# Optimization experiments

Hardware: AMD Instinct MI355X
Metric: run time of the kernel (lower is better)

## Reference

```python
import jax, jax.numpy as jnp
import numpy as np

V, M, E, H = 20000, 32, 128, 4      # vocab, max news per word, embed dim, heads
N, L, C = 8192, 64, 128             # num news, max sent len, cnn out channels
KS = (3, 4, 5)


def setup_inputs() -> dict:
    key = jax.random.key(0)
    ks = jax.random.split(key, 12)
    s = 0.02
    return {
        "word2news": jax.random.randint(ks[0], (V, M), 0, N),
        "word2news_len": jax.random.randint(ks[1], (V,), 0, M),
        "news_words": jax.random.randint(ks[2], (N, L), 0, V),
        "news_embed_table": jax.random.normal(ks[3], (N, E), jnp.float32) * s,
        "in_proj_w": jax.random.normal(ks[4], (3 * E, E), jnp.float32) * s,
        "in_proj_b": jnp.zeros((3 * E,), jnp.float32),
        "out_proj_w": jax.random.normal(ks[5], (E, E), jnp.float32) * s,
        "out_proj_b": jnp.zeros((E,), jnp.float32),
        "conv_w3": jax.random.normal(ks[6], (C, E, 3), jnp.float32) * s,
        "conv_b3": jnp.zeros((C,), jnp.float32),
        "conv_w4": jax.random.normal(ks[7], (C, E, 4), jnp.float32) * s,
        "conv_b4": jnp.zeros((C,), jnp.float32),
        "conv_w5": jax.random.normal(ks[8], (C, E, 5), jnp.float32) * s,
        "conv_b5": jnp.zeros((C,), jnp.float32),
        "fc_w": jax.random.normal(ks[9], (E, len(KS) * C), jnp.float32) * s,
        "fc_b": jnp.zeros((E,), jnp.float32),
    }


def _conv1d(x, w, b):
    # x: [N, E, L]  w: [C, E, k]  -> [N, C, L-k+1]
    y = jax.lax.conv_general_dilated(x, w, (1,), "VALID",
                                     dimension_numbers=("NCH", "OIH", "NCH"))
    return y + b[None, :, None]


def _word_embeds(word2news, word2news_len, table, in_w, in_b, out_w, out_b):
    # Batched version of the per-word loop: masked mean query + 1-query MHA.
    mask = jnp.arange(M)[None, :] < word2news_len[:, None]          # [V, M]
    ctx = table[word2news]                                           # [V, M, E]
    cnt = jnp.maximum(word2news_len, 1).astype(ctx.dtype)[:, None]
    q = jnp.sum(jnp.where(mask[:, :, None], ctx, 0.0), axis=1) / cnt  # [V, E]
    wq, wk, wv = jnp.split(in_w, 3, axis=0)
    bq, bk, bv = jnp.split(in_b, 3, axis=0)
    Dh = E // H
    qh = (q @ wq.T + bq).reshape(V, H, Dh)
    kh = (ctx @ wk.T + bk).reshape(V, M, H, Dh)
    vh = (ctx @ wv.T + bv).reshape(V, M, H, Dh)
    scores = jnp.einsum("vhd,vmhd->vhm", qh, kh) / jnp.sqrt(jnp.asarray(Dh, ctx.dtype))
    scores = jnp.where(mask[:, None, :], scores, -1e9)
    attn = jax.nn.softmax(scores, axis=-1)
    o = jnp.einsum("vhm,vmhd->vhd", attn, vh).reshape(V, E)
    o = o @ out_w.T + out_b
    # words with no news stay zero, matching the zeros-init table in torch
    return jnp.where((word2news_len > 0)[:, None], o, 0.0)            # [V, E]


def reference(word2news, word2news_len, news_words, news_embed_table,
              in_proj_w, in_proj_b, out_proj_w, out_proj_b,
              conv_w3, conv_b3, conv_w4, conv_b4, conv_w5, conv_b5,
              fc_w, fc_b):
    word_embeds = _word_embeds(word2news, word2news_len, news_embed_table,
                               in_proj_w, in_proj_b, out_proj_w, out_proj_b)
    doc = word_embeds[news_words]                 # [N, L, E]
    x = doc.transpose(0, 2, 1)                    # [N, E, L]
    pooled = [jnp.max(jax.nn.relu(_conv1d(x, w, b)), axis=2)
              for w, b in ((conv_w3, conv_b3), (conv_w4, conv_b4), (conv_w5, conv_b5))]
    feats = jnp.concatenate(pooled, axis=1)       # [N, 3*C]; dropout=identity (eval)
    return feats @ fc_w.T + fc_b                  # [N, E]
```

## Files before the change

kernel.cpp:

```cpp
#include <hip/hip_runtime.h>
#include <math.h>

#define V_WORDS 20000
#define MM 32
#define EE 128
#define HH 4
#define DHH 32
#define NN 8192
#define LL 64
#define CC 128

typedef short bf16x8 __attribute__((ext_vector_type(8)));
typedef float f32x4 __attribute__((ext_vector_type(4)));
typedef unsigned short u16;
typedef unsigned int u32;

__device__ __forceinline__ u16 f2bf(float x) {
    u32 u = __float_as_uint(x);
    u32 r = (u + 0x7FFFu + ((u >> 16) & 1u)) >> 16;
    return (u16)r;
}
__device__ __forceinline__ float bflo(u32 u) { return __uint_as_float(u << 16); }
__device__ __forceinline__ float bfhi(u32 u) { return __uint_as_float(u & 0xFFFF0000u); }

#if defined(__has_builtin)
#  if __has_builtin(__builtin_amdgcn_fdot2_f32_bf16)
#    define USE_BF16_DOT2 1
#  endif
#endif
#ifdef USE_BF16_DOT2
typedef __bf16 v2bf __attribute__((ext_vector_type(2)));
#endif

__device__ __forceinline__ float dot2bf(u32 a, u32 b, float c) {
#ifdef USE_BF16_DOT2
    return __builtin_amdgcn_fdot2_f32_bf16(
        __builtin_bit_cast(v2bf, a), __builtin_bit_cast(v2bf, b), c, false);
#else
    return c + bflo(a) * bflo(b) + bfhi(a) * bfhi(b);
#endif
}

__global__ __launch_bounds__(256)
void pack_weights(const float* __restrict__ w3,
                  const float* __restrict__ w4,
                  const float* __restrict__ w5,
                  u16* __restrict__ Bpack)
{
    const int s = blockIdx.x;
    const int t = threadIdx.x;
    const int lane = t & 63;

    const float* src;
    int K, sl;
    if (s < 12)      { src = w3; K = 3; sl = s; }
    else if (s < 28) { src = w4; K = 4; sl = s - 12; }
    else             { src = w5; K = 5; sl = s - 28; }
    const int j  = sl >> 2;
    const int e0 = (sl & 3) * 32;

    for (int nt = (t >> 6); nt < 8; nt += 4) {
        const int c = nt * 16 + (lane & 15);
        const int kb = (lane >> 4) * 8;
        u16 vals[8];
        #pragma unroll
        for (int i = 0; i < 8; ++i) {
            const int e = e0 + kb + i;
            vals[i] = f2bf(src[(c * EE + e) * K + j]);
        }
        u16* dst = Bpack + (((size_t)s * 8 + nt) * 64 + lane) * 8;
        *(bf16x8*)dst = *(const bf16x8*)vals;
    }
}

__global__ __launch_bounds__(256)
void kv_proj_kernel(const float* __restrict__ table,
                    const float* __restrict__ in_w,
                    const float* __restrict__ in_b,
                    u16* __restrict__ Kn16, u16* __restrict__ Vn16)
{
    const int n0 = blockIdx.x * 8;
    const int t = threadIdx.x;
    __shared__ float tbl[8][EE];
    {
        const int r = t >> 5, q4 = (t & 31) * 4;
        *(float4*)&tbl[r][q4] = *(const float4*)&table[(size_t)(n0 + r) * EE + q4];
    }
    __syncthreads();

    const int sel = t >> 7;
    const int i = t & 127;
    const float* w = in_w + (size_t)(sel + 1) * EE * EE + (size_t)i * EE;
    const float bias = in_b[(sel + 1) * EE + i];

    float acc[8];
    #pragma unroll
    for (int r = 0; r < 8; ++r) acc[r] = bias;
    for (int k = 0; k < EE; k += 4) {
        const float4 wv = *(const float4*)&w[k];
        #pragma unroll
        for (int r = 0; r < 8; ++r) {
            acc[r] += tbl[r][k]     * wv.x + tbl[r][k + 1] * wv.y
                    + tbl[r][k + 2] * wv.z + tbl[r][k + 3] * wv.w;
        }
    }
    u16* dst = sel ? Vn16 : Kn16;
    #pragma unroll
    for (int r = 0; r < 8; ++r) dst[(size_t)(n0 + r) * EE + i] = f2bf(acc[r]);
}

__global__ __launch_bounds__(384)
void kvqw_proj_kernel(const float* __restrict__ table,
                      const float* __restrict__ in_w,
                      const float* __restrict__ in_b,
                      const float* __restrict__ out_w,
                      const float* __restrict__ out_b,
                      u16* __restrict__ Qn16,
                      u16* __restrict__ Kn16,
                      u16* __restrict__ Wn16)
{
    const int n0 = blockIdx.x * 8;
    const int t = threadIdx.x;
    __shared__ float tbl[8][EE];
    __shared__ float vsh[8][EE];
    if (t < 256) {
        const int r = t >> 5, q4 = (t & 31) * 4;
        *(float4*)&tbl[r][q4] = *(const float4*)&table[(size_t)(n0 + r) * EE + q4];
    }
    __syncthreads();

    const int sel = t >> 7;
    const int i = t & 127;
    const float* w = in_w + (size_t)sel * EE * EE + (size_t)i * EE;
    const float bias = in_b[sel * EE + i];

    float acc[8];
    #pragma unroll
    for (int r = 0; r < 8; ++r) acc[r] = bias;
    for (int k = 0; k < EE; k += 4) {
        const float4 wv = *(const float4*)&w[k];
        #pragma unroll
        for (int r = 0; r < 8; ++r) {
            acc[r] += tbl[r][k]     * wv.x + tbl[r][k + 1] * wv.y
                    + tbl[r][k + 2] * wv.z + tbl[r][k + 3] * wv.w;
        }
    }
    if (sel == 0) {
        #pragma unroll
        for (int r = 0; r < 8; ++r) Qn16[(size_t)(n0 + r) * EE + i] = f2bf(acc[r]);
    } else if (sel == 1) {
        #pragma unroll
        for (int r = 0; r < 8; ++r) Kn16[(size_t)(n0 + r) * EE + i] = f2bf(acc[r]);
    } else {
        #pragma unroll
        for (int r = 0; r < 8; ++r) vsh[r][i] = acc[r];
    }
    __syncthreads();

    {
        const int g = t >> 7;
        const int r0 = g, r1 = g + 3, r2 = g + 6;
        const int r2c = (r2 < 8) ? r2 : 7;
        const float* wr = out_w + (size_t)i * EE;
        const float ob = out_b[i];
        float a0 = ob, a1 = ob, a2 = ob;
        #pragma unroll 4
        for (int k = 0; k < EE; k += 4) {
            const float4 wv = *(const float4*)&wr[k];
            a0 += vsh[r0][k]   * wv.x + vsh[r0][k+1] * wv.y
                + vsh[r0][k+2] * wv.z + vsh[r0][k+3] * wv.w;
            a1 += vsh[r1][k]   * wv.x + vsh[r1][k+1] * wv.y
                + vsh[r1][k+2] * wv.z + vsh[r1][k+3] * wv.w;
            a2 += vsh[r2c][k]   * wv.x + vsh[r2c][k+1] * wv.y
                + vsh[r2c][k+2] * wv.z + vsh[r2c][k+3] * wv.w;
        }
        Wn16[(size_t)(n0 + r0) * EE + i] = f2bf(a0);
        Wn16[(size_t)(n0 + r1) * EE + i] = f2bf(a1);
        if (r2 < 8) Wn16[(size_t)(n0 + r2) * EE + i] = f2bf(a2);
    }
}

#define WPB 8
__global__ __launch_bounds__(256, 3)
void word_attn_kernel(const int* __restrict__ word2news,
                      const int* __restrict__ word2news_len,
                      const float* __restrict__ table,
                      const float* __restrict__ in_w,
                      const float* __restrict__ in_b,
                      const float* __restrict__ out_w,
                      const float* __restrict__ out_b,
                      const u16* __restrict__ Kn16,
                      const u16* __restrict__ Vn16,
                      u16* __restrict__ we16)
{
    const int v0 = blockIdx.x * WPB;
    const int t = threadIdx.x;

    __shared__ int   rows[WPB][MM];
    __shared__ int   lenS[WPB];
    __shared__ float q[WPB][EE];
    __shared__ float qh[WPB][EE];
    __shared__ float attn[WPB][HH][MM];
    __shared__ float osh[WPB][EE];

    {
        const int w = t >> 5, m = t & 31;
        rows[w][m] = word2news[(size_t)(v0 + w) * MM + m];
        if (t < WPB) lenS[t] = word2news_len[v0 + t];
    }
    __syncthreads();

    {
        const int w = t >> 5, d0 = (t & 31) * 4;
        const int L = lenS[w];
        float4 a = {0.f, 0.f, 0.f, 0.f};
        #pragma unroll 4
        for (int m = 0; m < MM; ++m) {
            const float4 x = *(const float4*)&table[(size_t)rows[w][m] * EE + d0];
            if (m < L) { a.x += x.x; a.y += x.y; a.z += x.z; a.w += x.w; }
        }
        const float inv = (L > 0) ? 1.0f / (float)L : 0.0f;
        a.x *= inv; a.y *= inv; a.z *= inv; a.w *= inv;
        *(float4*)&q[w][d0] = a;
    }
    __syncthreads();

    {
        const int g = t >> 7, i = t & 127;
        const float* wr = in_w + (size_t)i * EE;
        float acc[4] = {0.f, 0.f, 0.f, 0.f};
        #pragma unroll 4
        for (int k = 0; k < EE; k += 4) {
            const float4 wv = *(const float4*)&wr[k];
            #pragma unroll
            for (int w4 = 0; w4 < 4; ++w4) {
                const float* qw = q[g * 4 + w4];
                acc[w4] += qw[k] * wv.x + qw[k + 1] * wv.y
                         + qw[k + 2] * wv.z + qw[k + 3] * wv.w;
            }
        }
        const float b = in_b[i];
        #pragma unroll
        for (int w4 = 0; w4 < 4; ++w4) qh[g * 4 + w4][i] = acc[w4] + b;
    }
    __syncthreads();

    {
        const int w = t >> 5, m = t & 31;
        const int L = lenS[w];
        float s[HH] = {-1e9f, -1e9f, -1e9f, -1e9f};
        if (m < L) {
            const uint4* kr = (const uint4*)(Kn16 + (size_t)rows[w][m] * EE);
            #pragma unroll 1
            for (int h = 0; h < HH; ++h) {
                float a = 0.f;
                #pragma unroll
                for (int k8 = 0; k8 < 4; ++k8) {
                    const uint4 u = kr[h * 4 + k8];
                    const float4 q0 = *(const float4*)&qh[w][h * 32 + k8 * 8];
                    const float4 q1 = *(const float4*)&qh[w][h * 32 + k8 * 8 + 4];
                    a += q0.x * bflo(u.x) + q0.y * bfhi(u.x)
                       + q0.z * bflo(u.y) + q0.w * bfhi(u.y)
                       + q1.x * bflo(u.z) + q1.y * bfhi(u.z)
                       + q1.z * bflo(u.w) + q1.w * bfhi(u.w);
                }
                s[h] = a * 0.17677669529663687f;
            }
        }
        #pragma unroll
        for (int h = 0; h < HH; ++h) {
            float mx = s[h];
            #pragma unroll
            for (int off = 16; off > 0; off >>= 1)
                mx = fmaxf(mx, __shfl_xor(mx, off, 32));
            const float ex = expf(s[h] - mx);
            float sum = ex;
            #pragma unroll
            for (int off = 16; off > 0; off >>= 1)
                sum += __shfl_xor(sum, off, 32);
            attn[w][h][m] = ex / sum;
        }
    }
    __syncthreads();

    {
        const int w = t >> 5, d0 = (t & 31) * 4;
        const int h = d0 >> 5;
        float4 a = {0.f, 0.f, 0.f, 0.f};
        #pragma unroll 4
        for (int m = 0; m < MM; ++m) {
            const float aw = attn[w][h][m];
            const u32* vr = (const u32*)(Vn16 + (size_t)rows[w][m] * EE + d0);
            const u32 u0 = vr[0], u1 = vr[1];
            a.x += aw * bflo(u0); a.y += aw * bfhi(u0);
            a.z += aw * bflo(u1); a.w += aw * bfhi(u1);
        }
        *(float4*)&osh[w][d0] = a;
    }
    __syncthreads();

    {
        const int g = t >> 7, i = t & 127;
        const float* wr = out_w + (size_t)i * EE;
        float acc[4] = {0.f, 0.f, 0.f, 0.f};
        #pragma unroll 4
        for (int k = 0; k < EE; k += 4) {
            const float4 wv = *(const float4*)&wr[k];
            #pragma unroll
            for (int w4 = 0; w4 < 4; ++w4) {
                const float* ow = osh[g * 4 + w4];
                acc[w4] += ow[k] * wv.x + ow[k + 1] * wv.y
                         + ow[k + 2] * wv.z + ow[k + 3] * wv.w;
            }
        }
        const float b = out_b[i];
        #pragma unroll
        for (int w4 = 0; w4 < 4; ++w4) {
            const int w = g * 4 + w4;
            we16[(size_t)(v0 + w) * EE + i] =
                (lenS[w] > 0) ? f2bf(acc[w4] + b) : (u16)0;
        }
    }
}

__global__ __launch_bounds__(256, 3)
void word_attn_wn(const int* __restrict__ word2news,
                  const int* __restrict__ word2news_len,
                  const u16* __restrict__ Qn16,
                  const u16* __restrict__ Kn16,
                  const u16* __restrict__ Wn16,
                  u16* __restrict__ we16)
{
    const int v0 = blockIdx.x * WPB;
    const int t = threadIdx.x;

    __shared__ int   rows[WPB][MM];
    __shared__ int   lenS[WPB];
    __shared__ __align__(16) u32 qhp[WPB][EE / 2];
    __shared__ float attn[WPB][HH][MM];

    {
        const int w = t >> 5, m = t & 31;
        rows[w][m] = word2news[(size_t)(v0 + w) * MM + m];
        if (t < WPB) lenS[t] = word2news_len[v0 + t];
    }
    __syncthreads();

    {
        const int w = t >> 5, d0 = (t & 31) * 4;
        const int L = lenS[w];
        float4 a = {0.f, 0.f, 0.f, 0.f};
        #pragma unroll 4
        for (int mm = 0; mm < L; ++mm) {
            const uint2 u = *(const uint2*)(Qn16 + (size_t)rows[w][mm] * EE + d0);
            a.x += bflo(u.x); a.y += bfhi(u.x);
            a.z += bflo(u.y); a.w += bfhi(u.y);
        }
        const float inv = (L > 0) ? 1.0f / (float)L : 0.0f;
        a.x *= inv; a.y *= inv; a.z *= inv; a.w *= inv;
        qhp[w][(d0 >> 1) + 0] = (u32)f2bf(a.x) | ((u32)f2bf(a.y) << 16);
        qhp[w][(d0 >> 1) + 1] = (u32)f2bf(a.z) | ((u32)f2bf(a.w) << 16);
    }
    __syncthreads();

    {
        const int w = t >> 5, m = t & 31;
        const int L = lenS[w];
        float s[HH] = {-1e9f, -1e9f, -1e9f, -1e9f};
        if (m < L) {
            const uint4* kr = (const uint4*)(Kn16 + (size_t)rows[w][m] * EE);
            const u32* qp = qhp[w];
            #pragma unroll
            for (int hp = 0; hp < 2; ++hp) {
                uint4 kq[8];
                #pragma unroll
                for (int q8 = 0; q8 < 8; ++q8) kq[q8] = kr[hp * 8 + q8];
                #pragma unroll
                for (int hl = 0; hl < 2; ++hl) {
                    const int h = hp * 2 + hl;
                    float a = 0.f;
                    #pragma unroll
                    for (int k8 = 0; k8 < 4; ++k8) {
                        const uint4 u  = kq[hl * 4 + k8];
                        const uint4 qq = *(const uint4*)&qp[h * 16 + k8 * 4];
                        a = dot2bf(u.x, qq.x, a);
                        a = dot2bf(u.y, qq.y, a);
                        a = dot2bf(u.z, qq.z, a);
                        a = dot2bf(u.w, qq.w, a);
                    }
                    s[h] = a * 0.17677669529663687f;
                }
            }
        }
        #pragma unroll
        for (int h = 0; h < HH; ++h) {
            float mx = s[h];
            #pragma unroll
            for (int off = 16; off > 0; off >>= 1)
                mx = fmaxf(mx, __shfl_xor(mx, off, 32));
            const float ex = __expf(s[h] - mx);
            float sum = ex;
            #pragma unroll
            for (int off = 16; off > 0; off >>= 1)
                sum += __shfl_xor(sum, off, 32);
            attn[w][h][m] = ex / sum;
        }
    }
    __syncthreads();

    {
        const int w = t >> 5, d0 = (t & 31) * 4;
        const int h = d0 >> 5;
        const int L = lenS[w];
        float4 a = {0.f, 0.f, 0.f, 0.f};
        #pragma unroll 4
        for (int mm = 0; mm < L; ++mm) {
            const float aw = attn[w][h][mm];
            const uint2 u = *(const uint2*)(Wn16 + (size_t)rows[w][mm] * EE + d0);
            a.x += aw * bflo(u.x); a.y += aw * bfhi(u.x);
            a.z += aw * bflo(u.y); a.w += aw * bfhi(u.y);
        }
        u32 lo = 0u, hi = 0u;
        if (L > 0) {
            lo = (u32)f2bf(a.x) | ((u32)f2bf(a.y) << 16);
            hi = (u32)f2bf(a.z) | ((u32)f2bf(a.w) << 16);
        }
        u32* dst = (u32*)(we16 + (size_t)(v0 + w) * EE + d0);
        dst[0] = lo; dst[1] = hi;
    }
}

#define DSTRIDE 136
#define DOCSZ   (68 * DSTRIDE)

template<int NSL, int SBASE, int NP>
__device__ __forceinline__ void conv_g2(const u16* __restrict__ lds,
                                        const u16* __restrict__ Bpack,
                                        const float* __restrict__ bk,
                                        int p, int nth, int l,
                                        float (&mxout)[4])
{
    f32x4 acc[4][4];
    #pragma unroll
    for (int mt = 0; mt < 4; ++mt)
        #pragma unroll
        for (int k = 0; k < 4; ++k)
            acc[mt][k] = (f32x4){0.f, 0.f, 0.f, 0.f};

    const int lm = l & 15;
    const int g  = l >> 4;
    const u16* bbase = Bpack + ((size_t)SBASE * 8 + nth * 4) * 512 + l * 8;
    const u16* abase = lds + (size_t)p * DOCSZ;

    #pragma unroll 2
    for (int s = 0; s < NSL; ++s) {
        const int j  = s >> 2;
        const int e0 = (s & 3) * 32;

        bf16x8 b[4];
        #pragma unroll
        for (int k = 0; k < 4; ++k)
            b[k] = *(const bf16x8*)(bbase + s * 4096 + k * 512);

        const u16* arow = abase + (lm + j) * DSTRIDE + e0 + g * 8;
        bf16x8 a[4];
        #pragma unroll
        for (int mt = 0; mt < 4; ++mt)
            a[mt] = *(const bf16x8*)(arow + mt * (16 * DSTRIDE));

        #pragma unroll
        for (int mt = 0; mt < 4; ++mt)
            #pragma unroll
            for (int k = 0; k < 4; ++k)
                acc[mt][k] = __builtin_amdgcn_mfma_f32_16x16x32_bf16(a[mt], b[k], acc[mt][k], 0, 0, 0);
    }

    #pragma unroll
    for (int k = 0; k < 4; ++k) {
        const int c = nth * 64 + k * 16 + lm;
        const float bias = bk[c];
        float mx = 0.0f;
        #pragma unroll
        for (int mt = 0; mt < 4; ++mt) {
            #pragma unroll
            for (int r = 0; r < 4; ++r) {
                const int pos = 16 * mt + g * 4 + r;
                const float y = fmaxf(acc[mt][k][r] + bias, 0.0f);
                if (pos < NP) mx = fmaxf(mx, y);
            }
        }
        mx = fmaxf(mx, __shfl_xor(mx, 16));
        mx = fmaxf(mx, __shfl_xor(mx, 32));
        mxout[k] = mx;
    }
}

__global__ __launch_bounds__(512, 4)
void news_kernel(const int* __restrict__ news_words,
                 const u16* __restrict__ we16,
                 const u16* __restrict__ Bpack,
                 const float* __restrict__ b3,
                 const float* __restrict__ b4,
                 const float* __restrict__ b5,
                 const float* __restrict__ fcw, const float* __restrict__ fcb,
                 float* __restrict__ out)
{
    const int n0 = blockIdx.x * 4;
    const int t = threadIdx.x;
    const int w = t >> 6, l = t & 63;
    const int p = w >> 1, nth = w & 1;

    __shared__ u16 lds[4 * DOCSZ];
    __shared__ int rows[4 * LL];

    if (t < 4 * LL) rows[t] = news_words[(size_t)n0 * LL + t];
    __syncthreads();

    {
        const uint4* weU = (const uint4*)we16;
        uint4* ldsU = (uint4*)lds;
        for (int idx = t; idx < 4096; idx += 512) {
            const int d = idx >> 10, rem = idx & 1023;
            const int row = rem >> 4, c4 = rem & 15;
            ldsU[d * 1156 + row * 17 + c4] = weU[(size_t)rows[d * 64 + row] * 16 + c4];
        }
        if (t < 256) {
            const int d = t >> 6, rem = t & 63;
            const int row = 64 + (rem >> 4), c4 = rem & 15;
            ldsU[d * 1156 + row * 17 + c4] = (uint4){0u, 0u, 0u, 0u};
        }
    }
    __syncthreads();

    float m3[4], m4[4], m5[4];
    conv_g2<12,  0, 62>(lds, Bpack, b3, p, nth, l, m3);
    conv_g2<16, 12, 61>(lds, Bpack, b4, p, nth, l, m4);
    conv_g2<20, 28, 60>(lds, Bpack, b5, p, nth, l, m5);
    __syncthreads();

    float* feats = (float*)lds;
    if ((l >> 4) == 0) {
        const int lm = l & 15;
        #pragma unroll
        for (int k = 0; k < 4; ++k) {
            const int c = nth * 64 + k * 16 + lm;
            feats[p * 384 +   0 + c] = m3[k];
            feats[p * 384 + 128 + c] = m4[k];
            feats[p * 384 + 256 + c] = m5[k];
        }
    }
    __syncthreads();

    if (t < 128) {
        const float4* wr4 = (const float4*)(fcw + (size_t)t * (3 * CC));
        float a0 = fcb[t], a1 = a0, a2 = a0, a3 = a0;
        for (int f4 = 0; f4 < 96; ++f4) {
            const float4 wv = wr4[f4];
            const float4 x0 = *(const float4*)&feats[0 * 384 + f4 * 4];
            const float4 x1 = *(const float4*)&feats[1 * 384 + f4 * 4];
            const float4 x2 = *(const float4*)&feats[2 * 384 + f4 * 4];
            const float4 x3 = *(const float4*)&feats[3 * 384 + f4 * 4];
            a0 += x0.x * wv.x + x0.y * wv.y + x0.z * wv.z + x0.w * wv.w;
            a1 += x1.x * wv.x + x1.y * wv.y + x1.z * wv.z + x1.w * wv.w;
            a2 += x2.x * wv.x + x2.y * wv.y + x2.z * wv.z + x2.w * wv.w;
            a3 += x3.x * wv.x + x3.y * wv.y + x3.z * wv.z + x3.w * wv.w;
        }
        out[(size_t)(n0 + 0) * EE + t] = a0;
        out[(size_t)(n0 + 1) * EE + t] = a1;
        out[(size_t)(n0 + 2) * EE + t] = a2;
        out[(size_t)(n0 + 3) * EE + t] = a3;
    }
}

extern "C" void kernel_launch(void* const* d_in, const int* in_sizes, int n_in,
                              void* d_out, int out_size, void* d_ws, size_t ws_size,
                              hipStream_t stream)
{
    const int*   word2news     = (const int*)d_in[0];
    const int*   word2news_len = (const int*)d_in[1];
    const int*   news_words    = (const int*)d_in[2];
    const float* table         = (const float*)d_in[3];
    const float* in_w          = (const float*)d_in[4];
    const float* in_b          = (const float*)d_in[5];
    const float* out_w         = (const float*)d_in[6];
    const float* out_b         = (const float*)d_in[7];
    const float* w3            = (const float*)d_in[8];
    const float* b3            = (const float*)d_in[9];
    const float* w4            = (const float*)d_in[10];
    const float* b4            = (const float*)d_in[11];
    const float* w5            = (const float*)d_in[12];
    const float* b5            = (const float*)d_in[13];
    const float* fcw           = (const float*)d_in[14];
    const float* fcb           = (const float*)d_in[15];

    float* out = (float*)d_out;
    u16* base  = (u16*)d_ws;
    u16* we16  = base;
    u16* Bpack = base + 2560000;
    u16* Kn16  = base + 2756608;
    u16* Wn16  = base + 3805184;
    u16* Qn16  = base + 4853760;
    const size_t need_qn = (size_t)(4853760 + 1048576) * 2;

    pack_weights<<<48, 256, 0, stream>>>(w3, w4, w5, Bpack);

    if (ws_size >= need_qn) {
        kvqw_proj_kernel<<<NN / 8, 384, 0, stream>>>(table, in_w, in_b,
                                                     out_w, out_b,
                                                     Qn16, Kn16, Wn16);
        word_attn_wn<<<V_WORDS / WPB, 256, 0, stream>>>(
            word2news, word2news_len, Qn16, Kn16, Wn16, we16);
    } else {
        kv_proj_kernel<<<NN / 8, 256, 0, stream>>>(table, in_w, in_b, Kn16, Wn16);
        word_attn_kernel<<<V_WORDS / WPB, 256, 0, stream>>>(
            word2news, word2news_len, table, in_w, in_b, out_w, out_b,
            Kn16, Wn16, we16);
    }

    news_kernel<<<NN / 4, 512, 0, stream>>>(
        news_words, we16, Bpack, b3, b4, b5, fcw, fcb, out);
}
```

Baseline: 371.7 us.

## Split conv MFMA work across position halves instead of channel halves

Each wave pair per document now splits the sequence positions into two 32-row halves and computes all 128 output channels, where before it split the channels into two 64-wide halves and covered all 64 positions. Per K-step each wave loads 8 B fragments from global or cache and 2 A fragments from LDS, instead of 4 of each. This cuts LDS reads but doubles the weight-fragment traffic. The max-pool is then combined across the two waves through shared memory, which adds an extra barrier and a read-modify-write.

Measured after the change: 435.5 us. 17.2% more time.

```diff
diff --git a/kernel.cpp b/kernel.cpp
--- a/kernel.cpp
+++ b/kernel.cpp
@@ -434,57 +434,56 @@
 #define DOCSZ   (68 * DSTRIDE)
 
 template<int NSL, int SBASE, int NP>
-__device__ __forceinline__ void conv_g2(const u16* __restrict__ lds,
+__device__ __forceinline__ void conv_mt(const u16* __restrict__ lds,
                                         const u16* __restrict__ Bpack,
                                         const float* __restrict__ bk,
-                                        int p, int nth, int l,
-                                        float (&mxout)[4])
-{
-    f32x4 acc[4][4];
+                                        int p, int mh, int l,
+                                        float (&mxout)[8])
+{
+    f32x4 acc[2][8];
     #pragma unroll
-    for (int mt = 0; mt < 4; ++mt)
-        #pragma unroll
-        for (int k = 0; k < 4; ++k)
+    for (int mt = 0; mt < 2; ++mt)
+        #pragma unroll
+        for (int k = 0; k < 8; ++k)
             acc[mt][k] = (f32x4){0.f, 0.f, 0.f, 0.f};
 
     const int lm = l & 15;
     const int g  = l >> 4;
-    const u16* bbase = Bpack + ((size_t)SBASE * 8 + nth * 4) * 512 + l * 8;
-    const u16* abase = lds + (size_t)p * DOCSZ;
+    const u16* bbase = Bpack + (size_t)SBASE * 8 * 512 + l * 8;
+    const u16* abase = lds + (size_t)p * DOCSZ + mh * (32 * DSTRIDE);
 
     #pragma unroll 2
     for (int s = 0; s < NSL; ++s) {
         const int j  = s >> 2;
         const int e0 = (s & 3) * 32;
 
-        bf16x8 b[4];
-        #pragma unroll
-        for (int k = 0; k < 4; ++k)
+        bf16x8 b[8];
+        #pragma unroll
+        for (int k = 0; k < 8; ++k)
             b[k] = *(const bf16x8*)(bbase + s * 4096 + k * 512);
 
         const u16* arow = abase + (lm + j) * DSTRIDE + e0 + g * 8;
-        bf16x8 a[4];
-        #pragma unroll
-        for (int mt = 0; mt < 4; ++mt)
+        bf16x8 a[2];
+        #pragma unroll
+        for (int mt = 0; mt < 2; ++mt)
             a[mt] = *(const bf16x8*)(arow + mt * (16 * DSTRIDE));
 
         #pragma unroll
-        for (int mt = 0; mt < 4; ++mt)
-            #pragma unroll
-            for (int k = 0; k < 4; ++k)
+        for (int mt = 0; mt < 2; ++mt)
+            #pragma unroll
+            for (int k = 0; k < 8; ++k)
                 acc[mt][k] = __builtin_amdgcn_mfma_f32_16x16x32_bf16(a[mt], b[k], acc[mt][k], 0, 0, 0);
     }
 
     #pragma unroll
-    for (int k = 0; k < 4; ++k) {
-        const int c = nth * 64 + k * 16 + lm;
-        const float bias = bk[c];
+    for (int k = 0; k < 8; ++k) {
+        const float bias = bk[k * 16 + lm];
         float mx = 0.0f;
         #pragma unroll
-        for (int mt = 0; mt < 4; ++mt) {
+        for (int mt = 0; mt < 2; ++mt) {
             #pragma unroll
             for (int r = 0; r < 4; ++r) {
-                const int pos = 16 * mt + g * 4 + r;
+                const int pos = mh * 32 + 16 * mt + g * 4 + r;
                 const float y = fmaxf(acc[mt][k][r] + bias, 0.0f);
                 if (pos < NP) mx = fmaxf(mx, y);
             }
@@ -508,7 +507,7 @@
     const int n0 = blockIdx.x * 4;
     const int t = threadIdx.x;
     const int w = t >> 6, l = t & 63;
-    const int p = w >> 1, nth = w & 1;
+    const int p = w >> 1, mh = w & 1;
 
     __shared__ u16 lds[4 * DOCSZ];
     __shared__ int rows[4 * LL];
@@ -532,21 +531,30 @@
     }
     __syncthreads();
 
-    float m3[4], m4[4], m5[4];
-    conv_g2<12,  0, 62>(lds, Bpack, b3, p, nth, l, m3);
-    conv_g2<16, 12, 61>(lds, Bpack, b4, p, nth, l, m4);
-    conv_g2<20, 28, 60>(lds, Bpack, b5, p, nth, l, m5);
+    float m3[8], m4[8], m5[8];
+    conv_mt<12,  0, 62>(lds, Bpack, b3, p, mh, l, m3);
+    conv_mt<16, 12, 61>(lds, Bpack, b4, p, mh, l, m4);
+    conv_mt<20, 28, 60>(lds, Bpack, b5, p, mh, l, m5);
     __syncthreads();
 
     float* feats = (float*)lds;
-    if ((l >> 4) == 0) {
-        const int lm = l & 15;
-        #pragma unroll
-        for (int k = 0; k < 4; ++k) {
-            const int c = nth * 64 + k * 16 + lm;
+    if (mh == 1 && l < 16) {
+        #pragma unroll
+        for (int k = 0; k < 8; ++k) {
+            const int c = k * 16 + l;
             feats[p * 384 +   0 + c] = m3[k];
             feats[p * 384 + 128 + c] = m4[k];
             feats[p * 384 + 256 + c] = m5[k];
+        }
+    }
+    __syncthreads();
+    if (mh == 0 && l < 16) {
+        #pragma unroll
+        for (int k = 0; k < 8; ++k) {
+            const int c = k * 16 + l;
+            feats[p * 384 +   0 + c] = fmaxf(feats[p * 384 +   0 + c], m3[k]);
+            feats[p * 384 + 128 + c] = fmaxf(feats[p * 384 + 128 + c], m4[k]);
+            feats[p * 384 + 256 + c] = fmaxf(feats[p * 384 + 256 + c], m5[k]);
         }
     }
     __syncthreads();
```
